# Kernel tuning notes

Hardware: AMD Instinct MI355X
Metric: run time of the kernel (lower is better)

Reference implementation:

```python
import jax, jax.numpy as jnp
import numpy as np


def log_g(x):
    # log of g(x) = where(x>=0, x+0.5, sigmoid(x)), computed stably in log space
    return jnp.where(x >= 0, jnp.log(jax.nn.relu(x) + 0.5), -jax.nn.softplus(-x))


def setup_inputs() -> dict:
    key = jax.random.key(0)
    k1, k2, k3, k4 = jax.random.split(key, 4)
    B, S, D, Di = 4, 8192, 512, 1024
    X = jax.random.normal(k1, (B, S, D), dtype=jnp.float32)
    # prev_hidden must be strictly positive (its log is taken)
    hidden = jax.random.uniform(k2, (B, 1, Di), dtype=jnp.float32) * 0.9 + 0.1
    W_hg = jax.random.normal(k3, (2 * Di, D), dtype=jnp.float32) * 0.02
    W_out = jax.random.normal(k4, (D, Di), dtype=jnp.float32) * 0.02
    return {"X": X, "hidden": hidden, "W_hg": W_hg, "W_out": W_out}


def reference(X, hidden, W_hg, W_out):
    # X: [B,S,D]; hidden: [B,1,Di]; W_hg: [2Di,D]; W_out: [D,Di]
    S = X.shape[1]
    hg = jnp.einsum('bsd,ed->bse', X, W_hg)            # [B,S,2Di]
    h, gate = jnp.split(hg, 2, axis=-1)                # each [B,S,Di]

    log_coeffs = -jax.nn.softplus(gate)                # log(1 - z)
    log_z = -jax.nn.softplus(-gate)                    # log z
    log_values = log_z + log_g(h)                      # log(z * g(h_tilde))

    # prepend prev hidden state
    log_values = jnp.concatenate([jnp.log(hidden), log_values], axis=1)  # [B,S+1,Di]
    log_coeffs = jnp.pad(log_coeffs, ((0, 0), (1, 0), (0, 0)))           # [B,S+1,Di]

    # Heinsen associative scan in log space
    a_star = jnp.cumsum(log_coeffs, axis=1)
    log_h = a_star + jax.lax.cumlogsumexp(log_values - a_star, axis=1)
    h_all = jnp.exp(log_h)[:, -S:]                     # [B,S,Di]

    next_prev_hidden = h_all[:, -1:]                   # [B,1,Di]
    out = jnp.einsum('bsi,di->bsd', h_all, W_out)      # [B,S,D]
    return out, next_prev_hidden
```

## Files before the change

### kernel.cpp

```cpp
#include <hip/hip_runtime.h>
#include <hip/hip_bf16.h>
#include <stdint.h>

typedef __attribute__((ext_vector_type(8))) short short8;
typedef __attribute__((ext_vector_type(4))) float f32x4;

#define CH 32
#define NC 256

__device__ __forceinline__ unsigned short f2bf(float f) {
  union { float f; unsigned u; } x; x.f = f;
  unsigned u = x.u;
  u = (u + 0x7fffu + ((u >> 16) & 1u)) >> 16;
  return (unsigned short)u;
}
__device__ __forceinline__ float bf2f(unsigned short h) {
  union { unsigned u; float f; } x; x.u = ((unsigned)h) << 16;
  return x.f;
}

__device__ __forceinline__ void store1(float* p, float v) { *p = v; }
__device__ __forceinline__ void store1(unsigned short* p, float v) { *p = f2bf(v); }
__device__ __forceinline__ float4 ld4(const float* p, size_t idx4) {
  return reinterpret_cast<const float4*>(p)[idx4];
}
__device__ __forceinline__ float4 ld4(const unsigned short* p, size_t idx4) {
  ushort4 u = reinterpret_cast<const ushort4*>(p)[idx4];
  return make_float4(bf2f(u.x), bf2f(u.y), bf2f(u.z), bf2f(u.w));
}

#define GLOAD_LDS16(gptr, lptr) \
  __builtin_amdgcn_global_load_lds((const __attribute__((address_space(1))) void*)(gptr), \
                                   (__attribute__((address_space(3))) void*)(lptr), 16, 0, 0)

__global__ void k_f32_to_bf16(const float* __restrict__ src, unsigned short* __restrict__ dst, int n4) {
  int i = blockIdx.x * blockDim.x + threadIdx.x;
  if (i >= n4) return;
  float4 f = reinterpret_cast<const float4*>(src)[i];
  ushort4 o = make_ushort4(f2bf(f.x), f2bf(f.y), f2bf(f.z), f2bf(f.w));
  reinterpret_cast<ushort4*>(dst)[i] = o;
}

template <typename TS>
__global__ __launch_bounds__(256, 2) void k_gemm1(
    const unsigned short* __restrict__ Xb,
    const unsigned short* __restrict__ Wb,
    TS* __restrict__ aArr, TS* __restrict__ vArr)
{
  __shared__ unsigned short As[128 * 64];
  __shared__ unsigned short Bs0[128 * 64];
  __shared__ unsigned short Bs1[128 * 64];

  const int m0 = blockIdx.y * 128;
  const int i0 = blockIdx.x * 128;
  const int tid = threadIdx.x;
  const int lane = tid & 63;
  const int wave = tid >> 6;
  const int wm = (wave >> 1) * 64;
  const int wn = (wave & 1) * 64;
  const int srow = tid >> 3;
  const int scol = (tid & 7) * 8;

  f32x4 acc0[4][4], acc1[4][4];
#pragma unroll
  for (int f = 0; f < 4; ++f)
#pragma unroll
    for (int g = 0; g < 4; ++g) {
      acc0[f][g] = f32x4{0.f, 0.f, 0.f, 0.f};
      acc1[f][g] = f32x4{0.f, 0.f, 0.f, 0.f};
    }

  for (int k0 = 0; k0 < 512; k0 += 64) {
    __syncthreads();
#pragma unroll
    for (int j = 0; j < 4; ++j) {
      int row = j * 32 + srow;
      GLOAD_LDS16(Xb + (size_t)(m0 + row) * 512 + k0 + scol, As + row * 64 + scol);
    }
#pragma unroll
    for (int j = 0; j < 4; ++j) {
      int row = j * 32 + srow;
      GLOAD_LDS16(Wb + (size_t)(i0 + row) * 512 + k0 + scol, Bs0 + row * 64 + scol);
    }
#pragma unroll
    for (int j = 0; j < 4; ++j) {
      int row = j * 32 + srow;
      GLOAD_LDS16(Wb + (size_t)(1024 + i0 + row) * 512 + k0 + scol, Bs1 + row * 64 + scol);
    }
    __syncthreads();

#pragma unroll
    for (int kk = 0; kk < 2; ++kk) {
      const int kof = kk * 32 + (lane >> 4) * 8;
      const int rl = lane & 15;
      short8 av[4], b0[4], b1[4];
#pragma unroll
      for (int f = 0; f < 4; ++f)
        av[f] = *(const short8*)(As + (wm + f * 16 + rl) * 64 + kof);
#pragma unroll
      for (int g = 0; g < 4; ++g) {
        b0[g] = *(const short8*)(Bs0 + (wn + g * 16 + rl) * 64 + kof);
        b1[g] = *(const short8*)(Bs1 + (wn + g * 16 + rl) * 64 + kof);
      }
#pragma unroll
      for (int f = 0; f < 4; ++f)
#pragma unroll
        for (int g = 0; g < 4; ++g) {
          acc0[f][g] = __builtin_amdgcn_mfma_f32_16x16x32_bf16(av[f], b0[g], acc0[f][g], 0, 0, 0);
          acc1[f][g] = __builtin_amdgcn_mfma_f32_16x16x32_bf16(av[f], b1[g], acc1[f][g], 0, 0, 0);
        }
    }
  }

  const int rl = lane & 15;
  const int rr = (lane >> 4) * 4;
#pragma unroll
  for (int f = 0; f < 4; ++f) {
#pragma unroll
    for (int g = 0; g < 4; ++g) {
#pragma unroll
      for (int r = 0; r < 4; ++r) {
        int m = m0 + wm + f * 16 + rr + r;
        int i = i0 + wn + g * 16 + rl;
        float h    = acc0[f][g][r];
        float gate = acc1[f][g][r];
        float e  = __expf(gate);
        float ac = 1.f / (1.f + e);
        float z  = e / (1.f + e);
        float gg = (h >= 0.f) ? (h + 0.5f) : (1.f / (1.f + __expf(-h)));
        size_t off = (size_t)m * 1024 + i;
        store1(aArr + off, ac);
        store1(vArr + off, z * gg);
      }
    }
  }
}

template <typename TS>
__global__ void k_scanA(const TS* __restrict__ aArr, const TS* __restrict__ vArr,
                        float* __restrict__ Acar, float* __restrict__ Vcar)
{
  int c = blockIdx.x & (NC - 1);
  int b = blockIdx.x >> 8;
  size_t base4 = (((size_t)b * 8192 + (size_t)c * CH) * 1024) / 4 + threadIdx.x;
  float4 A = make_float4(1.f, 1.f, 1.f, 1.f);
  float4 V = make_float4(0.f, 0.f, 0.f, 0.f);
#pragma unroll 4
  for (int t = 0; t < CH; ++t) {
    float4 at = ld4(aArr, base4 + (size_t)t * 256);
    float4 vt = ld4(vArr, base4 + (size_t)t * 256);
    V.x = fmaf(at.x, V.x, vt.x); V.y = fmaf(at.y, V.y, vt.y);
    V.z = fmaf(at.z, V.z, vt.z); V.w = fmaf(at.w, V.w, vt.w);
    A.x *= at.x; A.y *= at.y; A.z *= at.z; A.w *= at.w;
  }
  size_t co = (((size_t)b * NC + c) * 1024) / 4 + threadIdx.x;
  reinterpret_cast<float4*>(Acar)[co] = A;
  reinterpret_cast<float4*>(Vcar)[co] = V;
}

__global__ void k_scanB(const float* __restrict__ hidden,
                        const float* __restrict__ Acar, const float* __restrict__ Vcar,
                        float* __restrict__ Hstart)
{
  int t = blockIdx.x * blockDim.x + threadIdx.x;
  int b = t >> 10, i = t & 1023;
  float H = hidden[(size_t)b * 1024 + i];
  for (int c = 0; c < NC; ++c) {
    size_t o = ((size_t)b * NC + c) * 1024 + i;
    Hstart[o] = H;
    H = fmaf(Acar[o], H, Vcar[o]);
  }
}

template <typename TS>
__global__ void k_scanC(const TS* __restrict__ aArr, const TS* __restrict__ vArr,
                        const float* __restrict__ Hstart,
                        unsigned short* __restrict__ hAll, float* __restrict__ nextH)
{
  int c = blockIdx.x & (NC - 1);
  int b = blockIdx.x >> 8;
  size_t base4 = (((size_t)b * 8192 + (size_t)c * CH) * 1024) / 4 + threadIdx.x;
  size_t ho = (((size_t)b * NC + c) * 1024) / 4 + threadIdx.x;
  float4 H = reinterpret_cast<const float4*>(Hstart)[ho];
#pragma unroll 4
  for (int t = 0; t < CH; ++t) {
    float4 at = ld4(aArr, base4 + (size_t)t * 256);
    float4 vt = ld4(vArr, base4 + (size_t)t * 256);
    H.x = fmaf(at.x, H.x, vt.x); H.y = fmaf(at.y, H.y, vt.y);
    H.z = fmaf(at.z, H.z, vt.z); H.w = fmaf(at.w, H.w, vt.w);
    ushort4 o = make_ushort4(f2bf(H.x), f2bf(H.y), f2bf(H.z), f2bf(H.w));
    reinterpret_cast<ushort4*>(hAll)[base4 + (size_t)t * 256] = o;
  }
  if (c == NC - 1)
    reinterpret_cast<float4*>(nextH)[(size_t)b * 256 + threadIdx.x] = H;
}

__global__ __launch_bounds__(256, 2) void k_gemm2(
    const unsigned short* __restrict__ Ab,
    const unsigned short* __restrict__ Bb,
    float* __restrict__ out)
{
  __shared__ unsigned short As[128 * 64];
  __shared__ unsigned short Bs[128 * 64];

  const int m0 = blockIdx.y * 128;
  const int n0 = blockIdx.x * 128;
  const int tid = threadIdx.x;
  const int lane = tid & 63;
  const int wave = tid >> 6;
  const int wm = (wave >> 1) * 64;
  const int wn = (wave & 1) * 64;
  const int srow = tid >> 3;
  const int scol = (tid & 7) * 8;

  f32x4 acc[4][4];
#pragma unroll
  for (int f = 0; f < 4; ++f)
#pragma unroll
    for (int g = 0; g < 4; ++g) acc[f][g] = f32x4{0.f, 0.f, 0.f, 0.f};

  for (int k0 = 0; k0 < 1024; k0 += 64) {
    __syncthreads();
#pragma unroll
    for (int j = 0; j < 4; ++j) {
      int row = j * 32 + srow;
      GLOAD_LDS16(Ab + (size_t)(m0 + row) * 1024 + k0 + scol, As + row * 64 + scol);
    }
#pragma unroll
    for (int j = 0; j < 4; ++j) {
      int row = j * 32 + srow;
      GLOAD_LDS16(Bb + (size_t)(n0 + row) * 1024 + k0 + scol, Bs + row * 64 + scol);
    }
    __syncthreads();

#pragma unroll
    for (int kk = 0; kk < 2; ++kk) {
      const int kof = kk * 32 + (lane >> 4) * 8;
      const int rl = lane & 15;
      short8 av[4], bv[4];
#pragma unroll
      for (int f = 0; f < 4; ++f)
        av[f] = *(const short8*)(As + (wm + f * 16 + rl) * 64 + kof);
#pragma unroll
      for (int g = 0; g < 4; ++g)
        bv[g] = *(const short8*)(Bs + (wn + g * 16 + rl) * 64 + kof);
#pragma unroll
      for (int f = 0; f < 4; ++f)
#pragma unroll
        for (int g = 0; g < 4; ++g)
          acc[f][g] = __builtin_amdgcn_mfma_f32_16x16x32_bf16(av[f], bv[g], acc[f][g], 0, 0, 0);
    }
  }

  const int rl = lane & 15;
  const int rr = (lane >> 4) * 4;
#pragma unroll
  for (int f = 0; f < 4; ++f)
#pragma unroll
    for (int g = 0; g < 4; ++g)
#pragma unroll
      for (int r = 0; r < 4; ++r) {
        int m = m0 + wm + f * 16 + rr + r;
        int n = n0 + wn + g * 16 + rl;
        out[(size_t)m * 512 + n] = acc[f][g][r];
      }
}

template <typename TS>
static void run_pipeline(const float* X, const float* hidden, const float* W_hg,
                         const float* W_out, float* out, float* nextH,
                         unsigned short* Xb, unsigned short* Whgb, unsigned short* Woutb,
                         unsigned short* hAll, float* Acar, float* Vcar, float* Hstart,
                         TS* aArr, TS* vArr, hipStream_t stream)
{
  k_f32_to_bf16<<<16384, 256, 0, stream>>>(X, Xb, 16777216 / 4);
  k_f32_to_bf16<<<1024, 256, 0, stream>>>(W_hg, Whgb, 1048576 / 4);
  k_f32_to_bf16<<<512, 256, 0, stream>>>(W_out, Woutb, 524288 / 4);

  dim3 g1(8, 256);
  k_gemm1<TS><<<g1, 256, 0, stream>>>(Xb, Whgb, aArr, vArr);

  k_scanA<TS><<<4 * NC, 256, 0, stream>>>(aArr, vArr, Acar, Vcar);
  k_scanB<<<16, 256, 0, stream>>>(hidden, Acar, Vcar, Hstart);
  k_scanC<TS><<<4 * NC, 256, 0, stream>>>(aArr, vArr, Hstart, hAll, nextH);

  dim3 g2(4, 256);
  k_gemm2<<<g2, 256, 0, stream>>>(hAll, Woutb, out);
}

extern "C" void kernel_launch(void* const* d_in, const int* in_sizes, int n_in,
                              void* d_out, int out_size, void* d_ws, size_t ws_size,
                              hipStream_t stream) {
  const float* X      = (const float*)d_in[0];
  const float* hidden = (const float*)d_in[1];
  const float* W_hg   = (const float*)d_in[2];
  const float* W_out  = (const float*)d_in[3];

  float* out   = (float*)d_out;
  float* nextH = out + (size_t)32768 * 512;

  char* ws = (char*)d_ws;
  size_t off = 0;
  auto alloc = [&](size_t bytes) -> void* {
    void* p = ws + off;
    off = (off + bytes + 255) & ~(size_t)255;
    return p;
  };
  unsigned short* Xb    = (unsigned short*)alloc(32768ULL * 512 * 2);
  unsigned short* Whgb  = (unsigned short*)alloc(2048ULL * 512 * 2);
  unsigned short* Woutb = (unsigned short*)alloc(512ULL * 1024 * 2);
  unsigned short* hAll  = (unsigned short*)alloc(32768ULL * 1024 * 2);
  float* Acar   = (float*)alloc(4ULL * NC * 1024 * 4);
  float* Vcar   = (float*)alloc(4ULL * NC * 1024 * 4);
  float* Hstart = (float*)alloc(4ULL * NC * 1024 * 4);

  const size_t fixed = off;
  const size_t need_f32 = fixed + 2ULL * 32768ULL * 1024 * 4 + 512;

  if (ws_size >= need_f32) {
    float* aArr = (float*)alloc(32768ULL * 1024 * 4);
    float* vArr = (float*)alloc(32768ULL * 1024 * 4);
    run_pipeline<float>(X, hidden, W_hg, W_out, out, nextH,
                        Xb, Whgb, Woutb, hAll, Acar, Vcar, Hstart, aArr, vArr, stream);
  } else {
    unsigned short* aArr = (unsigned short*)alloc(32768ULL * 1024 * 2);
    unsigned short* vArr = (unsigned short*)alloc(32768ULL * 1024 * 2);
    run_pipeline<unsigned short>(X, hidden, W_hg, W_out, out, nextH,
                                 Xb, Whgb, Woutb, hAll, Acar, Vcar, Hstart, aArr, vArr, stream);
  }
}
```

Measured before the change: 371.6 us.

## Fuse chunk-carry scan into GEMM1 epilogue and pack coefficients as bf16 pairs

GEMM1's epilogue now computes each 64-row chunk's carry (A, V) directly from the accumulators, combining segments with cross-lane shuffles, so the separate scanA pass over the full coefficient arrays is gone. Coefficient and value are stored as one packed pair of bf16 values per element, read with a single wide load in scanC, replacing two separate (often fp32) arrays. Chunk size doubles to 64 (128 chunks) and launch bounds are raised to 3 blocks per CU. The risks are bf16 rounding of the stored coefficients, which compounds along the scan, and register pressure in the GEMM1 epilogue.

Measured after the change: 594.6 us. +60.0%, slower.

```diff
diff --git a/kernel.cpp b/kernel.cpp
--- a/kernel.cpp
+++ b/kernel.cpp
@@ -5,8 +5,8 @@
 typedef __attribute__((ext_vector_type(8))) short short8;
 typedef __attribute__((ext_vector_type(4))) float f32x4;
 
-#define CH 32
-#define NC 256
+#define CH 64
+#define NC 128
 
 __device__ __forceinline__ unsigned short f2bf(float f) {
   union { float f; unsigned u; } x; x.f = f;
@@ -14,19 +14,9 @@
   u = (u + 0x7fffu + ((u >> 16) & 1u)) >> 16;
   return (unsigned short)u;
 }
-__device__ __forceinline__ float bf2f(unsigned short h) {
-  union { unsigned u; float f; } x; x.u = ((unsigned)h) << 16;
+__device__ __forceinline__ float bf2f(unsigned u16) {
+  union { unsigned u; float f; } x; x.u = u16 << 16;
   return x.f;
-}
-
-__device__ __forceinline__ void store1(float* p, float v) { *p = v; }
-__device__ __forceinline__ void store1(unsigned short* p, float v) { *p = f2bf(v); }
-__device__ __forceinline__ float4 ld4(const float* p, size_t idx4) {
-  return reinterpret_cast<const float4*>(p)[idx4];
-}
-__device__ __forceinline__ float4 ld4(const unsigned short* p, size_t idx4) {
-  ushort4 u = reinterpret_cast<const ushort4*>(p)[idx4];
-  return make_float4(bf2f(u.x), bf2f(u.y), bf2f(u.z), bf2f(u.w));
 }
 
 #define GLOAD_LDS16(gptr, lptr) \
@@ -41,11 +31,11 @@
   reinterpret_cast<ushort4*>(dst)[i] = o;
 }
 
-template <typename TS>
-__global__ __launch_bounds__(256, 2) void k_gemm1(
+__global__ __launch_bounds__(256, 3) void k_gemm1(
     const unsigned short* __restrict__ Xb,
     const unsigned short* __restrict__ Wb,
-    TS* __restrict__ aArr, TS* __restrict__ vArr)
+    uint32_t* __restrict__ avArr,
+    float* __restrict__ Acar, float* __restrict__ Vcar)
 {
   __shared__ unsigned short As[128 * 64];
   __shared__ unsigned short Bs0[128 * 64];
@@ -113,49 +103,55 @@
   }
 
   const int rl = lane & 15;
-  const int rr = (lane >> 4) * 4;
-#pragma unroll
-  for (int f = 0; f < 4; ++f) {
-#pragma unroll
-    for (int g = 0; g < 4; ++g) {
+  const int q  = lane >> 4;
+  const int mb = m0 + wm;
+  const int b  = mb >> 13;
+  const int c  = (mb & 8191) >> 6;
+
+#pragma unroll
+  for (int g = 0; g < 4; ++g) {
+    const int i = i0 + wn + g * 16 + rl;
+    float Achunk = 1.f, Vchunk = 0.f;
+#pragma unroll
+    for (int f = 0; f < 4; ++f) {
+      float Aseg = 1.f, Vseg = 0.f;
 #pragma unroll
       for (int r = 0; r < 4; ++r) {
-        int m = m0 + wm + f * 16 + rr + r;
-        int i = i0 + wn + g * 16 + rl;
         float h    = acc0[f][g][r];
         float gate = acc1[f][g][r];
         float e  = __expf(gate);
-        float ac = 1.f / (1.f + e);
-        float z  = e / (1.f + e);
-        float gg = (h >= 0.f) ? (h + 0.5f) : (1.f / (1.f + __expf(-h)));
-        size_t off = (size_t)m * 1024 + i;
-        store1(aArr + off, ac);
-        store1(vArr + off, z * gg);
-      }
-    }
-  }
-}
-
-template <typename TS>
-__global__ void k_scanA(const TS* __restrict__ aArr, const TS* __restrict__ vArr,
-                        float* __restrict__ Acar, float* __restrict__ Vcar)
-{
-  int c = blockIdx.x & (NC - 1);
-  int b = blockIdx.x >> 8;
-  size_t base4 = (((size_t)b * 8192 + (size_t)c * CH) * 1024) / 4 + threadIdx.x;
-  float4 A = make_float4(1.f, 1.f, 1.f, 1.f);
-  float4 V = make_float4(0.f, 0.f, 0.f, 0.f);
-#pragma unroll 4
-  for (int t = 0; t < CH; ++t) {
-    float4 at = ld4(aArr, base4 + (size_t)t * 256);
-    float4 vt = ld4(vArr, base4 + (size_t)t * 256);
-    V.x = fmaf(at.x, V.x, vt.x); V.y = fmaf(at.y, V.y, vt.y);
-    V.z = fmaf(at.z, V.z, vt.z); V.w = fmaf(at.w, V.w, vt.w);
-    A.x *= at.x; A.y *= at.y; A.z *= at.z; A.w *= at.w;
-  }
-  size_t co = (((size_t)b * NC + c) * 1024) / 4 + threadIdx.x;
-  reinterpret_cast<float4*>(Acar)[co] = A;
-  reinterpret_cast<float4*>(Vcar)[co] = V;
+        float ac = __builtin_amdgcn_rcpf(1.f + e);
+        float z  = e * ac;
+        float gg;
+        if (h >= 0.f) gg = h + 0.5f;
+        else { float eh = __expf(h); gg = eh * __builtin_amdgcn_rcpf(1.f + eh); }
+        float v = z * gg;
+        int m = mb + f * 16 + q * 4 + r;
+        avArr[(size_t)m * 1024 + i] = (uint32_t)f2bf(ac) | ((uint32_t)f2bf(v) << 16);
+        Vseg = Vseg * ac + v;
+        Aseg = Aseg * ac;
+      }
+      {
+        float Ap = __shfl_xor(Aseg, 16);
+        float Vp = __shfl_xor(Vseg, 16);
+        if (q & 1) { Vseg = Vp * Aseg + Vseg; Aseg = Ap * Aseg; }
+        else       { Vseg = Vseg * Ap + Vp;   Aseg = Aseg * Ap; }
+      }
+      {
+        float Ap = __shfl_xor(Aseg, 32);
+        float Vp = __shfl_xor(Vseg, 32);
+        if (q & 2) { Vseg = Vp * Aseg + Vseg; Aseg = Ap * Aseg; }
+        else       { Vseg = Vseg * Ap + Vp;   Aseg = Aseg * Ap; }
+      }
+      Vchunk = Vchunk * Aseg + Vseg;
+      Achunk = Achunk * Aseg;
+    }
+    if (lane < 16) {
+      size_t co = ((size_t)b * NC + c) * 1024 + i;
+      Acar[co] = Achunk;
+      Vcar[co] = Vchunk;
+    }
+  }
 }
 
 __global__ void k_scanB(const float* __restrict__ hidden,
@@ -172,22 +168,22 @@
   }
 }
 
-template <typename TS>
-__global__ void k_scanC(const TS* __restrict__ aArr, const TS* __restrict__ vArr,
+__global__ void k_scanC(const uint32_t* __restrict__ av,
                         const float* __restrict__ Hstart,
                         unsigned short* __restrict__ hAll, float* __restrict__ nextH)
 {
   int c = blockIdx.x & (NC - 1);
-  int b = blockIdx.x >> 8;
+  int b = blockIdx.x >> 7;
   size_t base4 = (((size_t)b * 8192 + (size_t)c * CH) * 1024) / 4 + threadIdx.x;
   size_t ho = (((size_t)b * NC + c) * 1024) / 4 + threadIdx.x;
   float4 H = reinterpret_cast<const float4*>(Hstart)[ho];
 #pragma unroll 4
   for (int t = 0; t < CH; ++t) {
-    float4 at = ld4(aArr, base4 + (size_t)t * 256);
-    float4 vt = ld4(vArr, base4 + (size_t)t * 256);
-    H.x = fmaf(at.x, H.x, vt.x); H.y = fmaf(at.y, H.y, vt.y);
-    H.z = fmaf(at.z, H.z, vt.z); H.w = fmaf(at.w, H.w, vt.w);
+    uint4 u = reinterpret_cast<const uint4*>(av)[base4 + (size_t)t * 256];
+    H.x = fmaf(bf2f(u.x & 0xffffu), H.x, bf2f(u.x >> 16));
+    H.y = fmaf(bf2f(u.y & 0xffffu), H.y, bf2f(u.y >> 16));
+    H.z = fmaf(bf2f(u.z & 0xffffu), H.z, bf2f(u.z >> 16));
+    H.w = fmaf(bf2f(u.w & 0xffffu), H.w, bf2f(u.w >> 16));
     ushort4 o = make_ushort4(f2bf(H.x), f2bf(H.y), f2bf(H.z), f2bf(H.w));
     reinterpret_cast<ushort4*>(hAll)[base4 + (size_t)t * 256] = o;
   }
@@ -195,7 +191,7 @@
     reinterpret_cast<float4*>(nextH)[(size_t)b * 256 + threadIdx.x] = H;
 }
 
-__global__ __launch_bounds__(256, 2) void k_gemm2(
+__global__ __launch_bounds__(256, 3) void k_gemm2(
     const unsigned short* __restrict__ Ab,
     const unsigned short* __restrict__ Bb,
     float* __restrict__ out)
@@ -264,28 +260,6 @@
         int n = n0 + wn + g * 16 + rl;
         out[(size_t)m * 512 + n] = acc[f][g][r];
       }
-}
-
-template <typename TS>
-static void run_pipeline(const float* X, const float* hidden, const float* W_hg,
-                         const float* W_out, float* out, float* nextH,
-                         unsigned short* Xb, unsigned short* Whgb, unsigned short* Woutb,
-                         unsigned short* hAll, float* Acar, float* Vcar, float* Hstart,
-                         TS* aArr, TS* vArr, hipStream_t stream)
-{
-  k_f32_to_bf16<<<16384, 256, 0, stream>>>(X, Xb, 16777216 / 4);
-  k_f32_to_bf16<<<1024, 256, 0, stream>>>(W_hg, Whgb, 1048576 / 4);
-  k_f32_to_bf16<<<512, 256, 0, stream>>>(W_out, Woutb, 524288 / 4);
-
-  dim3 g1(8, 256);
-  k_gemm1<TS><<<g1, 256, 0, stream>>>(Xb, Whgb, aArr, vArr);
-
-  k_scanA<TS><<<4 * NC, 256, 0, stream>>>(aArr, vArr, Acar, Vcar);
-  k_scanB<<<16, 256, 0, stream>>>(hidden, Acar, Vcar, Hstart);
-  k_scanC<TS><<<4 * NC, 256, 0, stream>>>(aArr, vArr, Hstart, hAll, nextH);
-
-  dim3 g2(4, 256);
-  k_gemm2<<<g2, 256, 0, stream>>>(hAll, Woutb, out);
 }
 
 extern "C" void kernel_launch(void* const* d_in, const int* in_sizes, int n_in,
@@ -310,22 +284,21 @@
   unsigned short* Whgb  = (unsigned short*)alloc(2048ULL * 512 * 2);
   unsigned short* Woutb = (unsigned short*)alloc(512ULL * 1024 * 2);
   unsigned short* hAll  = (unsigned short*)alloc(32768ULL * 1024 * 2);
-  float* Acar   = (float*)alloc(4ULL * NC * 1024 * 4);
-  float* Vcar   = (float*)alloc(4ULL * NC * 1024 * 4);
-  float* Hstart = (float*)alloc(4ULL * NC * 1024 * 4);
-
-  const size_t fixed = off;
-  const size_t need_f32 = fixed + 2ULL * 32768ULL * 1024 * 4 + 512;
-
-  if (ws_size >= need_f32) {
-    float* aArr = (float*)alloc(32768ULL * 1024 * 4);
-    float* vArr = (float*)alloc(32768ULL * 1024 * 4);
-    run_pipeline<float>(X, hidden, W_hg, W_out, out, nextH,
-                        Xb, Whgb, Woutb, hAll, Acar, Vcar, Hstart, aArr, vArr, stream);
-  } else {
-    unsigned short* aArr = (unsigned short*)alloc(32768ULL * 1024 * 2);
-    unsigned short* vArr = (unsigned short*)alloc(32768ULL * 1024 * 2);
-    run_pipeline<unsigned short>(X, hidden, W_hg, W_out, out, nextH,
-                                 Xb, Whgb, Woutb, hAll, Acar, Vcar, Hstart, aArr, vArr, stream);
-  }
-}
+  float*    Acar   = (float*)alloc(4ULL * NC * 1024 * 4);
+  float*    Vcar   = (float*)alloc(4ULL * NC * 1024 * 4);
+  float*    Hstart = (float*)alloc(4ULL * NC * 1024 * 4);
+  uint32_t* avArr  = (uint32_t*)alloc(32768ULL * 1024 * 4);
+
+  k_f32_to_bf16<<<16384, 256, 0, stream>>>(X, Xb, 16777216 / 4);
+  k_f32_to_bf16<<<1024, 256, 0, stream>>>(W_hg, Whgb, 1048576 / 4);
+  k_f32_to_bf16<<<512, 256, 0, stream>>>(W_out, Woutb, 524288 / 4);
+
+  dim3 g1(8, 256);
+  k_gemm1<<<g1, 256, 0, stream>>>(Xb, Whgb, avArr, Acar, Vcar);
+
+  k_scanB<<<16, 256, 0, stream>>>(hidden, Acar, Vcar, Hstart);
+  k_scanC<<<4 * NC, 256, 0, stream>>>(avArr, Hstart, hAll, nextH);
+
+  dim3 g2(4, 256);
+  k_gemm2<<<g2, 256, 0, stream>>>(hAll, Woutb, out);
+}
```
